# Kernel tuning notes

Hardware: AMD Instinct MI355X
Metric: run time of the kernel (lower is better)

## Reference

```python
import jax, jax.numpy as jnp
import numpy as np

N_NODES = 50000
N_EDGES = 800000
D_IN, D_H1, D_H2 = 256, 128, 64


def setup_inputs() -> dict:
    key = jax.random.key(0)
    k1, k2, k3, k4, k5, k6, k7 = jax.random.split(key, 7)
    x = jax.random.normal(k1, (N_NODES, D_IN), dtype=jnp.float32)
    edge_index = jax.random.randint(k2, (2, N_EDGES), 0, N_NODES, dtype=jnp.int64)
    edge_weight = jax.random.uniform(k3, (N_EDGES,), dtype=jnp.float32)
    # GCNConv params: Linear (no bias) weight + separate bias, Glorot-ish scale
    W1 = jax.random.normal(k4, (D_IN, D_H1), dtype=jnp.float32) / np.sqrt(D_IN)
    b1 = jnp.zeros((D_H1,), dtype=jnp.float32)
    W2 = jax.random.normal(k5, (D_H1, D_H2), dtype=jnp.float32) / np.sqrt(D_H1)
    b2 = jnp.zeros((D_H2,), dtype=jnp.float32)
    return {"x": x, "edge_index": edge_index, "edge_weight": edge_weight,
            "W1": W1, "b1": b1, "W2": W2, "b2": b2}


def _gcn_norm(edge_index, edge_weight, n_nodes):
    # PyG gcn_norm: add self-loops (weight 1), symmetric D^-1/2 A D^-1/2
    loops = jnp.arange(n_nodes, dtype=edge_index.dtype)
    src = jnp.concatenate([edge_index[0], loops])
    dst = jnp.concatenate([edge_index[1], loops])
    w = jnp.concatenate([edge_weight, jnp.ones((n_nodes,), edge_weight.dtype)])
    deg = jax.ops.segment_sum(w, dst, num_segments=n_nodes)
    dinv = jnp.where(deg > 0, jax.lax.rsqrt(deg), 0.0)
    norm = dinv[src] * w * dinv[dst]  # [E+N]
    return src, dst, norm


def _gcn_conv(h, src, dst, norm, W, b, n_nodes):
    h = h @ W                                   # [N, d_out] dense GEMM
    msg = h[src] * norm[:, None]                # gather + scale  [E+N, d_out]
    out = jax.ops.segment_sum(msg, dst, num_segments=n_nodes)  # scatter-add
    return out + b


def reference(x, edge_index, edge_weight, W1, b1, W2, b2):
    n = x.shape[0]
    src, dst, norm = _gcn_norm(edge_index, edge_weight, n)
    # dropout p=0 -> identity
    h = jax.nn.relu(_gcn_conv(x, src, dst, norm, W1, b1, n))
    h = jax.nn.relu(_gcn_conv(h, src, dst, norm, W2, b2, n))
    return h
```

## Files before the change

### kernel.cpp

```cpp
#include <hip/hip_runtime.h>


static constexpr int SCAN_CHUNK = 1024;
static constexpr int CPAD = 16;

using short8 = __attribute__((ext_vector_type(8))) short;
using f32x4  = __attribute__((ext_vector_type(4))) float;

__device__ inline unsigned short bf16rne(float f) {
  unsigned u = __float_as_uint(f);
  u += 0x7fffu + ((u >> 16) & 1u);
  return (unsigned short)(u >> 16);
}
__device__ inline float bflo(unsigned u) { return __uint_as_float(u << 16); }
__device__ inline float bfhi(unsigned u) { return __uint_as_float(u & 0xffff0000u); }

__device__ inline void wtp_pack(const float* __restrict__ W,
                                unsigned short* __restrict__ Wtp,
                                int i, int K, int C) {
  int e = i & 7;
  int l = (i >> 3) & 63;
  int rest = i >> 9;
  int NT = C / 16;
  int nt = rest % NT;
  int kc = rest / NT;
  int k = kc * 32 + (l >> 4) * 8 + e;
  int n = nt * 16 + (l & 15);
  Wtp[i] = bf16rne(W[(size_t)k * C + n]);
}

__global__ __launch_bounds__(256) void k_prep(int* __restrict__ cnt, int nz,
                                              const float* __restrict__ W1,
                                              unsigned short* __restrict__ wtp1,
                                              const float* __restrict__ W2,
                                              unsigned short* __restrict__ wtp2) {
  int i = blockIdx.x * 256 + threadIdx.x;
  if (i < nz) cnt[i] = 0;
  if (i < 256 * 128) wtp_pack(W1, wtp1, i, 256, 128);
  if (i < 128 * 64) wtp_pack(W2, wtp2, i, 128, 64);
}

__global__ __launch_bounds__(256) void k_count(const int* __restrict__ dst,
                                               int* __restrict__ cnt,
                                               int* __restrict__ epos, int E) {
  const int base = blockIdx.x * 1024 + threadIdx.x;
  int d[4];
#pragma unroll
  for (int j = 0; j < 4; ++j) {
    int e = base + j * 256;
    d[j] = (e < E) ? dst[e] : -1;
  }
#pragma unroll
  for (int j = 0; j < 4; ++j) {
    int e = base + j * 256;
    if (e < E) epos[e] = atomicAdd(&cnt[(size_t)d[j] * CPAD], 1);
  }
}

__global__ __launch_bounds__(256) void k_scan1(const int* __restrict__ in,
                                               int* __restrict__ out,
                                               int* __restrict__ sums, int n) {
  __shared__ int sd[256];
  const int base = blockIdx.x * SCAN_CHUNK;
  const int tid = threadIdx.x;
  int v[4], tot = 0;
#pragma unroll
  for (int j = 0; j < 4; ++j) {
    int idx = base + tid * 4 + j;
    v[j] = (idx < n) ? in[(size_t)idx * CPAD] : 0;
    tot += v[j];
  }
  sd[tid] = tot;
  __syncthreads();
  for (int d = 1; d < 256; d <<= 1) {
    int t = (tid >= d) ? sd[tid - d] : 0;
    __syncthreads();
    sd[tid] += t;
    __syncthreads();
  }
  if (tid == 255) sums[blockIdx.x] = sd[255];
  int run = sd[tid] - tot;
#pragma unroll
  for (int j = 0; j < 4; ++j) {
    int idx = base + tid * 4 + j;
    if (idx < n) out[idx] = run;
    run += v[j];
  }
}

__global__ __launch_bounds__(64) void k_scan2(int* __restrict__ sums, int n) {
  int tid = threadIdx.x;
  int o = (tid < n) ? sums[tid] : 0;
  int v = o;
  for (int d = 1; d < 64; d <<= 1) {
    int t = __shfl_up(v, d, 64);
    if (tid >= d) v += t;
  }
  if (tid < n) sums[tid] = v - o;
}

__global__ __launch_bounds__(256) void k_scan3(int* __restrict__ out,
                                               const int* __restrict__ sums, int n) {
  const int base = blockIdx.x * SCAN_CHUNK;
  const int add = sums[blockIdx.x];
  for (int j = threadIdx.x; j < SCAN_CHUNK; j += 256) {
    int idx = base + j;
    if (idx < n) out[idx] += add;
  }
}

__global__ __launch_bounds__(256) void k_bucket2(const int* __restrict__ src,
                                                 const int* __restrict__ dst,
                                                 const float* __restrict__ w,
                                                 const int* __restrict__ row_ptr,
                                                 const int* __restrict__ epos,
                                                 int2* __restrict__ csr, int E) {
  int e = blockIdx.x * 256 + threadIdx.x;
  if (e < E) {
    int d = dst[e];
    csr[row_ptr[d] + epos[e]] = make_int2(src[e], __float_as_int(w[e]));
  }
}

__global__ __launch_bounds__(256) void k_deg_dinv(const int* __restrict__ row_ptr,
                                                  const int2* __restrict__ csr,
                                                  float* __restrict__ dinv, int n) {
  int i = blockIdx.x * 256 + threadIdx.x;
  if (i >= n) return;
  const int e0 = row_ptr[i], e1 = row_ptr[i + 1];
  float s = 1.0f;
  int e = e0;
  for (; e + 4 <= e1; e += 4) {
    float w0 = __int_as_float(csr[e].y), w1 = __int_as_float(csr[e + 1].y);
    float w2 = __int_as_float(csr[e + 2].y), w3 = __int_as_float(csr[e + 3].y);
    s += (w0 + w1) + (w2 + w3);
  }
  for (; e < e1; ++e) s += __int_as_float(csr[e].y);
  dinv[i] = rsqrtf(s);
}

template <int K, int C, bool A_F32>
__global__ __launch_bounds__(256, A_F32 ? 3 : 4) void k_gemm_mfma(
    const void* __restrict__ Aptr, const unsigned short* __restrict__ Wtp,
    const float* __restrict__ dinv, unsigned short* __restrict__ H, int n) {
  constexpr int NT = C / 16;
  constexpr int KCH = K / 32;
  const int w = threadIdx.x >> 6;
  const int l = threadIdx.x & 63;
  const int lm = l & 15;
  const int lk = (l >> 4) * 8;
  const int row0 = (blockIdx.x * 4 + w) * 16;
  if (row0 >= n) return;
  const int m = row0 + lm;
  const bool valid = m < n;
  const size_t arow = (size_t)(valid ? m : 0) * K;

  short8 af[KCH];
  if (A_F32) {
    const float* A = (const float*)Aptr;
    float4 a[2 * KCH];
#pragma unroll
    for (int c = 0; c < KCH; ++c) {
      if (valid) {
        a[2 * c]     = *(const float4*)(A + arow + c * 32 + lk);
        a[2 * c + 1] = *(const float4*)(A + arow + c * 32 + lk + 4);
      } else {
        a[2 * c] = a[2 * c + 1] = make_float4(0.f, 0.f, 0.f, 0.f);
      }
    }
#pragma unroll
    for (int c = 0; c < KCH; ++c) {
      af[c][0] = (short)bf16rne(a[2 * c].x);     af[c][1] = (short)bf16rne(a[2 * c].y);
      af[c][2] = (short)bf16rne(a[2 * c].z);     af[c][3] = (short)bf16rne(a[2 * c].w);
      af[c][4] = (short)bf16rne(a[2 * c + 1].x); af[c][5] = (short)bf16rne(a[2 * c + 1].y);
      af[c][6] = (short)bf16rne(a[2 * c + 1].z); af[c][7] = (short)bf16rne(a[2 * c + 1].w);
    }
  } else {
    const unsigned short* A = (const unsigned short*)Aptr;
#pragma unroll
    for (int c = 0; c < KCH; ++c)
      af[c] = valid ? *(const short8*)(A + arow + c * 32 + lk)
                    : short8{0, 0, 0, 0, 0, 0, 0, 0};
  }

  f32x4 acc[NT] = {};
  const short8* B = (const short8*)Wtp;
#pragma unroll
  for (int c = 0; c < KCH; ++c)
#pragma unroll
    for (int nt = 0; nt < NT; ++nt)
      acc[nt] = __builtin_amdgcn_mfma_f32_16x16x32_bf16(af[c], B[(c * NT + nt) * 64 + l],
                                                        acc[nt], 0, 0, 0);

  const int orow = row0 + (l >> 4) * 4;
  float dv[4];
#pragma unroll
  for (int r = 0; r < 4; ++r) dv[r] = (orow + r < n) ? dinv[orow + r] : 0.f;
#pragma unroll
  for (int nt = 0; nt < NT; ++nt) {
#pragma unroll
    for (int r = 0; r < 4; ++r) {
      int g = orow + r;
      if (g < n) H[(size_t)g * C + nt * 16 + lm] = bf16rne(acc[nt][r] * dv[r]);
    }
  }
}

template <int C, bool OUTF32>
__global__ __launch_bounds__(256) void k_aggregate(
    const int* __restrict__ row_ptr, const int2* __restrict__ csr,
    const unsigned short* __restrict__ h, const float* __restrict__ dinv,
    const float* __restrict__ bias, void* __restrict__ outp, int n) {
  constexpr int LPN = C / 8;
  constexpr int NPB = 256 / LPN;
  const int g = threadIdx.x % LPN;
  const int i = blockIdx.x * NPB + threadIdx.x / LPN;
  if (i >= n) return;
  const uint4* h4 = (const uint4*)h;
  uint4 hv = h4[(size_t)i * LPN + g];
  float a0 = bflo(hv.x), a1 = bfhi(hv.x), a2 = bflo(hv.y), a3 = bfhi(hv.y);
  float a4 = bflo(hv.z), a5 = bfhi(hv.z), a6 = bflo(hv.w), a7 = bfhi(hv.w);
  const int e1 = row_ptr[i + 1];
  int e = row_ptr[i];
  for (; e + 8 <= e1; e += 8) {
    int2 c[8];
    uint4 v[8];
#pragma unroll
    for (int j = 0; j < 8; ++j) c[j] = csr[e + j];
#pragma unroll
    for (int j = 0; j < 8; ++j) v[j] = h4[(size_t)c[j].x * LPN + g];
#pragma unroll
    for (int j = 0; j < 8; ++j) {
      float wj = __int_as_float(c[j].y);
      a0 = fmaf(bflo(v[j].x), wj, a0); a1 = fmaf(bfhi(v[j].x), wj, a1);
      a2 = fmaf(bflo(v[j].y), wj, a2); a3 = fmaf(bfhi(v[j].y), wj, a3);
      a4 = fmaf(bflo(v[j].z), wj, a4); a5 = fmaf(bfhi(v[j].z), wj, a5);
      a6 = fmaf(bflo(v[j].w), wj, a6); a7 = fmaf(bfhi(v[j].w), wj, a7);
    }
  }
  for (; e + 4 <= e1; e += 4) {
    int2 c[4];
    uint4 v[4];
#pragma unroll
    for (int j = 0; j < 4; ++j) c[j] = csr[e + j];
#pragma unroll
    for (int j = 0; j < 4; ++j) v[j] = h4[(size_t)c[j].x * LPN + g];
#pragma unroll
    for (int j = 0; j < 4; ++j) {
      float wj = __int_as_float(c[j].y);
      a0 = fmaf(bflo(v[j].x), wj, a0); a1 = fmaf(bfhi(v[j].x), wj, a1);
      a2 = fmaf(bflo(v[j].y), wj, a2); a3 = fmaf(bfhi(v[j].y), wj, a3);
      a4 = fmaf(bflo(v[j].z), wj, a4); a5 = fmaf(bfhi(v[j].z), wj, a5);
      a6 = fmaf(bflo(v[j].w), wj, a6); a7 = fmaf(bfhi(v[j].w), wj, a7);
    }
  }
  for (; e < e1; ++e) {
    int2 c = csr[e];
    float wj = __int_as_float(c.y);
    uint4 v = h4[(size_t)c.x * LPN + g];
    a0 = fmaf(bflo(v.x), wj, a0); a1 = fmaf(bfhi(v.x), wj, a1);
    a2 = fmaf(bflo(v.y), wj, a2); a3 = fmaf(bfhi(v.y), wj, a3);
    a4 = fmaf(bflo(v.z), wj, a4); a5 = fmaf(bfhi(v.z), wj, a5);
    a6 = fmaf(bflo(v.w), wj, a6); a7 = fmaf(bfhi(v.w), wj, a7);
  }
  const float di = dinv[i];
  const float4* b4 = (const float4*)bias;
  float4 bb0 = b4[g * 2], bb1 = b4[g * 2 + 1];
  a0 = fmaxf(fmaf(a0, di, bb0.x), 0.f); a1 = fmaxf(fmaf(a1, di, bb0.y), 0.f);
  a2 = fmaxf(fmaf(a2, di, bb0.z), 0.f); a3 = fmaxf(fmaf(a3, di, bb0.w), 0.f);
  a4 = fmaxf(fmaf(a4, di, bb1.x), 0.f); a5 = fmaxf(fmaf(a5, di, bb1.y), 0.f);
  a6 = fmaxf(fmaf(a6, di, bb1.z), 0.f); a7 = fmaxf(fmaf(a7, di, bb1.w), 0.f);
  if (OUTF32) {
    float4* o4 = (float4*)outp;
    o4[(size_t)i * (C / 4) + g * 2]     = make_float4(a0, a1, a2, a3);
    o4[(size_t)i * (C / 4) + g * 2 + 1] = make_float4(a4, a5, a6, a7);
  } else {
    uint4 o;
    o.x = (unsigned)bf16rne(a0) | ((unsigned)bf16rne(a1) << 16);
    o.y = (unsigned)bf16rne(a2) | ((unsigned)bf16rne(a3) << 16);
    o.z = (unsigned)bf16rne(a4) | ((unsigned)bf16rne(a5) << 16);
    o.w = (unsigned)bf16rne(a6) | ((unsigned)bf16rne(a7) << 16);
    ((uint4*)outp)[(size_t)i * LPN + g] = o;
  }
}

extern "C" void kernel_launch(void* const* d_in, const int* in_sizes, int n_in,
                              void* d_out, int out_size, void* d_ws, size_t ws_size,
                              hipStream_t stream) {
  (void)n_in; (void)out_size; (void)ws_size;
  const float* x  = (const float*)d_in[0];
  const int*   ei = (const int*)d_in[1];
  const float* ew = (const float*)d_in[2];
  const float* W1 = (const float*)d_in[3];
  const float* b1 = (const float*)d_in[4];
  const float* W2 = (const float*)d_in[5];
  const float* b2 = (const float*)d_in[6];
  float* out = (float*)d_out;

  const int N = in_sizes[0] / 256;
  const int E = in_sizes[2];
  const int* src = ei;
  const int* dst = ei + E;

  float* ws      = (float*)d_ws;
  float* dinv    = ws;
  int*   row_ptr = (int*)(ws + 50176);
  int*   chunks  = row_ptr + 50176;
  int*   cnt     = chunks + 256;
  int*   epos    = cnt + 800256;
  int2*  csr     = (int2*)(epos + 800256);
  unsigned short* h1   = (unsigned short*)((int*)csr + 2 * 800256);
  unsigned short* o1   = h1 + (size_t)50000 * 128;
  unsigned short* wtp1 = o1 + (size_t)50000 * 128;
  unsigned short* wtp2 = wtp1 + 128 * 256;
  unsigned short* h2   = h1;

  const int nz = (N + 1) * CPAD;
  const int nchunks = (N + 1 + SCAN_CHUNK - 1) / SCAN_CHUNK;

  k_prep<<<(nz + 255) / 256, 256, 0, stream>>>(cnt, nz, W1, wtp1, W2, wtp2);
  k_count<<<(E + 1023) / 1024, 256, 0, stream>>>(dst, cnt, epos, E);
  k_scan1<<<nchunks, 256, 0, stream>>>(cnt, row_ptr, chunks, N + 1);
  k_scan2<<<1, 64, 0, stream>>>(chunks, nchunks);
  k_scan3<<<nchunks, 256, 0, stream>>>(row_ptr, chunks, N + 1);
  k_bucket2<<<(E + 255) / 256, 256, 0, stream>>>(src, dst, ew, row_ptr, epos, csr, E);
  k_deg_dinv<<<(N + 255) / 256, 256, 0, stream>>>(row_ptr, csr, dinv, N);

  k_gemm_mfma<256, 128, true><<<(N + 63) / 64, 256, 0, stream>>>(x, wtp1, dinv, h1, N);
  k_aggregate<128, false><<<(N + 15) / 16, 256, 0, stream>>>(row_ptr, csr, h1, dinv,
                                                             b1, o1, N);
  k_gemm_mfma<128, 64, false><<<(N + 63) / 64, 256, 0, stream>>>(o1, wtp2, dinv, h2, N);
  k_aggregate<64, true><<<(N + 31) / 32, 256, 0, stream>>>(row_ptr, csr, h2, dinv,
                                                           b2, out, N);
}
```

Before: 154.2 us.

## Fuse layer-1 GEMM into count kernel, drop scan3, fold src dinv into edge weights

The first GEMM no longer depends on dinv: its blocks are appended to the edge-count launch so the MFMA work overlaps the atomic counting. The scan's third pass is removed, and consumers instead add the per-chunk offset when reading row_ptr. A new finalize pass multiplies each CSR edge weight by dinv[src], so aggregation scales only the self term by dinv[i]. This adds a pass over all edges and an extra offset lookup per row read, in exchange for removing a launch and the dinv scaling in the GEMM epilogue.

Result: no change. 151.3 us (-1.9%).

```diff
diff --git a/kernel.cpp b/kernel.cpp
--- a/kernel.cpp
+++ b/kernel.cpp
@@ -40,21 +40,73 @@
   if (i < 128 * 64) wtp_pack(W2, wtp2, i, 128, 64);
 }
 
-__global__ __launch_bounds__(256) void k_count(const int* __restrict__ dst,
-                                               int* __restrict__ cnt,
-                                               int* __restrict__ epos, int E) {
-  const int base = blockIdx.x * 1024 + threadIdx.x;
-  int d[4];
-#pragma unroll
-  for (int j = 0; j < 4; ++j) {
-    int e = base + j * 256;
-    d[j] = (e < E) ? dst[e] : -1;
-  }
-#pragma unroll
-  for (int j = 0; j < 4; ++j) {
-    int e = base + j * 256;
-    if (e < E) epos[e] = atomicAdd(&cnt[(size_t)d[j] * CPAD], 1);
-  }
+__global__ __launch_bounds__(256, 3) void k_count_gemm1(
+    const int* __restrict__ dst, int* __restrict__ cnt, int* __restrict__ epos,
+    int E, int CB,
+    const float* __restrict__ A, const unsigned short* __restrict__ Wtp,
+    unsigned short* __restrict__ H, int n) {
+  if (blockIdx.x < CB) {
+    const int base = blockIdx.x * 1024 + threadIdx.x;
+    int d[4];
+#pragma unroll
+    for (int j = 0; j < 4; ++j) {
+      int e = base + j * 256;
+      d[j] = (e < E) ? dst[e] : -1;
+    }
+#pragma unroll
+    for (int j = 0; j < 4; ++j) {
+      int e = base + j * 256;
+      if (e < E) epos[e] = atomicAdd(&cnt[(size_t)d[j] * CPAD], 1);
+    }
+    return;
+  }
+  constexpr int K = 256, C = 128, NT = C / 16, KCH = K / 32;
+  const int w = threadIdx.x >> 6;
+  const int l = threadIdx.x & 63;
+  const int lm = l & 15;
+  const int lk = (l >> 4) * 8;
+  const int row0 = ((blockIdx.x - CB) * 4 + w) * 16;
+  if (row0 >= n) return;
+  const int m = row0 + lm;
+  const bool valid = m < n;
+  const size_t arow = (size_t)(valid ? m : 0) * K;
+
+  short8 af[KCH];
+  {
+    float4 a[2 * KCH];
+#pragma unroll
+    for (int c = 0; c < KCH; ++c) {
+      if (valid) {
+        a[2 * c]     = *(const float4*)(A + arow + c * 32 + lk);
+        a[2 * c + 1] = *(const float4*)(A + arow + c * 32 + lk + 4);
+      } else {
+        a[2 * c] = a[2 * c + 1] = make_float4(0.f, 0.f, 0.f, 0.f);
+      }
+    }
+#pragma unroll
+    for (int c = 0; c < KCH; ++c) {
+      af[c][0] = (short)bf16rne(a[2 * c].x);     af[c][1] = (short)bf16rne(a[2 * c].y);
+      af[c][2] = (short)bf16rne(a[2 * c].z);     af[c][3] = (short)bf16rne(a[2 * c].w);
+      af[c][4] = (short)bf16rne(a[2 * c + 1].x); af[c][5] = (short)bf16rne(a[2 * c + 1].y);
+      af[c][6] = (short)bf16rne(a[2 * c + 1].z); af[c][7] = (short)bf16rne(a[2 * c + 1].w);
+    }
+  }
+  f32x4 acc[NT] = {};
+  const short8* B = (const short8*)Wtp;
+#pragma unroll
+  for (int c = 0; c < KCH; ++c)
+#pragma unroll
+    for (int nt = 0; nt < NT; ++nt)
+      acc[nt] = __builtin_amdgcn_mfma_f32_16x16x32_bf16(af[c], B[(c * NT + nt) * 64 + l],
+                                                        acc[nt], 0, 0, 0);
+  const int orow = row0 + (l >> 4) * 4;
+#pragma unroll
+  for (int nt = 0; nt < NT; ++nt)
+#pragma unroll
+    for (int r = 0; r < 4; ++r) {
+      int g = orow + r;
+      if (g < n) H[(size_t)g * C + nt * 16 + lm] = bf16rne(acc[nt][r]);
+    }
 }
 
 __global__ __launch_bounds__(256) void k_scan1(const int* __restrict__ in,
@@ -99,35 +151,29 @@
   if (tid < n) sums[tid] = v - o;
 }
 
-__global__ __launch_bounds__(256) void k_scan3(int* __restrict__ out,
-                                               const int* __restrict__ sums, int n) {
-  const int base = blockIdx.x * SCAN_CHUNK;
-  const int add = sums[blockIdx.x];
-  for (int j = threadIdx.x; j < SCAN_CHUNK; j += 256) {
-    int idx = base + j;
-    if (idx < n) out[idx] += add;
-  }
-}
-
 __global__ __launch_bounds__(256) void k_bucket2(const int* __restrict__ src,
                                                  const int* __restrict__ dst,
                                                  const float* __restrict__ w,
                                                  const int* __restrict__ row_ptr,
+                                                 const int* __restrict__ chunks,
                                                  const int* __restrict__ epos,
                                                  int2* __restrict__ csr, int E) {
   int e = blockIdx.x * 256 + threadIdx.x;
   if (e < E) {
     int d = dst[e];
-    csr[row_ptr[d] + epos[e]] = make_int2(src[e], __float_as_int(w[e]));
+    int pos = row_ptr[d] + chunks[d >> 10] + epos[e];
+    csr[pos] = make_int2(src[e], __float_as_int(w[e]));
   }
 }
 
 __global__ __launch_bounds__(256) void k_deg_dinv(const int* __restrict__ row_ptr,
+                                                  const int* __restrict__ chunks,
                                                   const int2* __restrict__ csr,
                                                   float* __restrict__ dinv, int n) {
   int i = blockIdx.x * 256 + threadIdx.x;
   if (i >= n) return;
-  const int e0 = row_ptr[i], e1 = row_ptr[i + 1];
+  const int e0 = row_ptr[i] + chunks[i >> 10];
+  const int e1 = row_ptr[i + 1] + chunks[(i + 1) >> 10];
   float s = 1.0f;
   int e = e0;
   for (; e + 4 <= e1; e += 4) {
@@ -139,12 +185,22 @@
   dinv[i] = rsqrtf(s);
 }
 
-template <int K, int C, bool A_F32>
-__global__ __launch_bounds__(256, A_F32 ? 3 : 4) void k_gemm_mfma(
-    const void* __restrict__ Aptr, const unsigned short* __restrict__ Wtp,
-    const float* __restrict__ dinv, unsigned short* __restrict__ H, int n) {
-  constexpr int NT = C / 16;
-  constexpr int KCH = K / 32;
+__global__ __launch_bounds__(256) void k_finalize(int2* __restrict__ csr,
+                                                  const float* __restrict__ dinv,
+                                                  int E) {
+  int e = blockIdx.x * 256 + threadIdx.x;
+  if (e < E) {
+    int2 c = csr[e];
+    c.y = __float_as_int(__int_as_float(c.y) * dinv[c.x]);
+    csr[e] = c;
+  }
+}
+
+template <int K, int C>
+__global__ __launch_bounds__(256, 4) void k_gemm_bf(
+    const unsigned short* __restrict__ A, const unsigned short* __restrict__ Wtp,
+    unsigned short* __restrict__ H, int n) {
+  constexpr int NT = C / 16, KCH = K / 32;
   const int w = threadIdx.x >> 6;
   const int l = threadIdx.x & 63;
   const int lm = l & 15;
@@ -154,35 +210,11 @@
   const int m = row0 + lm;
   const bool valid = m < n;
   const size_t arow = (size_t)(valid ? m : 0) * K;
-
   short8 af[KCH];
-  if (A_F32) {
-    const float* A = (const float*)Aptr;
-    float4 a[2 * KCH];
-#pragma unroll
-    for (int c = 0; c < KCH; ++c) {
-      if (valid) {
-        a[2 * c]     = *(const float4*)(A + arow + c * 32 + lk);
-        a[2 * c + 1] = *(const float4*)(A + arow + c * 32 + lk + 4);
-      } else {
-        a[2 * c] = a[2 * c + 1] = make_float4(0.f, 0.f, 0.f, 0.f);
-      }
-    }
-#pragma unroll
-    for (int c = 0; c < KCH; ++c) {
-      af[c][0] = (short)bf16rne(a[2 * c].x);     af[c][1] = (short)bf16rne(a[2 * c].y);
-      af[c][2] = (short)bf16rne(a[2 * c].z);     af[c][3] = (short)bf16rne(a[2 * c].w);
-      af[c][4] = (short)bf16rne(a[2 * c + 1].x); af[c][5] = (short)bf16rne(a[2 * c + 1].y);
-      af[c][6] = (short)bf16rne(a[2 * c + 1].z); af[c][7] = (short)bf16rne(a[2 * c + 1].w);
-    }
-  } else {
-    const unsigned short* A = (const unsigned short*)Aptr;
-#pragma unroll
-    for (int c = 0; c < KCH; ++c)
-      af[c] = valid ? *(const short8*)(A + arow + c * 32 + lk)
-                    : short8{0, 0, 0, 0, 0, 0, 0, 0};
-  }
-
+#pragma unroll
+  for (int c = 0; c < KCH; ++c)
+    af[c] = valid ? *(const short8*)(A + arow + c * 32 + lk)
+                  : short8{0, 0, 0, 0, 0, 0, 0, 0};
   f32x4 acc[NT] = {};
   const short8* B = (const short8*)Wtp;
 #pragma unroll
@@ -191,37 +223,36 @@
     for (int nt = 0; nt < NT; ++nt)
       acc[nt] = __builtin_amdgcn_mfma_f32_16x16x32_bf16(af[c], B[(c * NT + nt) * 64 + l],
                                                         acc[nt], 0, 0, 0);
-
   const int orow = row0 + (l >> 4) * 4;
-  float dv[4];
-#pragma unroll
-  for (int r = 0; r < 4; ++r) dv[r] = (orow + r < n) ? dinv[orow + r] : 0.f;
-#pragma unroll
-  for (int nt = 0; nt < NT; ++nt) {
+#pragma unroll
+  for (int nt = 0; nt < NT; ++nt)
 #pragma unroll
     for (int r = 0; r < 4; ++r) {
       int g = orow + r;
-      if (g < n) H[(size_t)g * C + nt * 16 + lm] = bf16rne(acc[nt][r] * dv[r]);
-    }
-  }
+      if (g < n) H[(size_t)g * C + nt * 16 + lm] = bf16rne(acc[nt][r]);
+    }
 }
 
 template <int C, bool OUTF32>
 __global__ __launch_bounds__(256) void k_aggregate(
-    const int* __restrict__ row_ptr, const int2* __restrict__ csr,
-    const unsigned short* __restrict__ h, const float* __restrict__ dinv,
-    const float* __restrict__ bias, void* __restrict__ outp, int n) {
+    const int* __restrict__ row_ptr, const int* __restrict__ chunks,
+    const int2* __restrict__ csr, const unsigned short* __restrict__ h,
+    const float* __restrict__ dinv, const float* __restrict__ bias,
+    void* __restrict__ outp, int n) {
   constexpr int LPN = C / 8;
   constexpr int NPB = 256 / LPN;
   const int g = threadIdx.x % LPN;
   const int i = blockIdx.x * NPB + threadIdx.x / LPN;
   if (i >= n) return;
+  const float di = dinv[i];
   const uint4* h4 = (const uint4*)h;
   uint4 hv = h4[(size_t)i * LPN + g];
-  float a0 = bflo(hv.x), a1 = bfhi(hv.x), a2 = bflo(hv.y), a3 = bfhi(hv.y);
-  float a4 = bflo(hv.z), a5 = bfhi(hv.z), a6 = bflo(hv.w), a7 = bfhi(hv.w);
-  const int e1 = row_ptr[i + 1];
-  int e = row_ptr[i];
+  float a0 = di * bflo(hv.x), a1 = di * bfhi(hv.x);
+  float a2 = di * bflo(hv.y), a3 = di * bfhi(hv.y);
+  float a4 = di * bflo(hv.z), a5 = di * bfhi(hv.z);
+  float a6 = di * bflo(hv.w), a7 = di * bfhi(hv.w);
+  const int e1 = row_ptr[i + 1] + chunks[(i + 1) >> 10];
+  int e = row_ptr[i] + chunks[i >> 10];
   for (; e + 8 <= e1; e += 8) {
     int2 c[8];
     uint4 v[8];
@@ -263,7 +294,6 @@
     a4 = fmaf(bflo(v.z), wj, a4); a5 = fmaf(bfhi(v.z), wj, a5);
     a6 = fmaf(bflo(v.w), wj, a6); a7 = fmaf(bfhi(v.w), wj, a7);
   }
-  const float di = dinv[i];
   const float4* b4 = (const float4*)bias;
   float4 bb0 = b4[g * 2], bb1 = b4[g * 2 + 1];
   a0 = fmaxf(fmaf(a0, di, bb0.x), 0.f); a1 = fmaxf(fmaf(a1, di, bb0.y), 0.f);
@@ -317,19 +347,21 @@
 
   const int nz = (N + 1) * CPAD;
   const int nchunks = (N + 1 + SCAN_CHUNK - 1) / SCAN_CHUNK;
+  const int CB = (E + 1023) / 1024;
+  const int GB = (N + 63) / 64;
 
   k_prep<<<(nz + 255) / 256, 256, 0, stream>>>(cnt, nz, W1, wtp1, W2, wtp2);
-  k_count<<<(E + 1023) / 1024, 256, 0, stream>>>(dst, cnt, epos, E);
+  k_count_gemm1<<<CB + GB, 256, 0, stream>>>(dst, cnt, epos, E, CB, x, wtp1, h1, N);
   k_scan1<<<nchunks, 256, 0, stream>>>(cnt, row_ptr, chunks, N + 1);
   k_scan2<<<1, 64, 0, stream>>>(chunks, nchunks);
-  k_scan3<<<nchunks, 256, 0, stream>>>(row_ptr, chunks, N + 1);
-  k_bucket2<<<(E + 255) / 256, 256, 0, stream>>>(src, dst, ew, row_ptr, epos, csr, E);
-  k_deg_dinv<<<(N + 255) / 256, 256, 0, stream>>>(row_ptr, csr, dinv, N);
-
-  k_gemm_mfma<256, 128, true><<<(N + 63) / 64, 256, 0, stream>>>(x, wtp1, dinv, h1, N);
-  k_aggregate<128, false><<<(N + 15) / 16, 256, 0, stream>>>(row_ptr, csr, h1, dinv,
-                                                             b1, o1, N);
-  k_gemm_mfma<128, 64, false><<<(N + 63) / 64, 256, 0, stream>>>(o1, wtp2, dinv, h2, N);
-  k_aggregate<64, true><<<(N + 31) / 32, 256, 0, stream>>>(row_ptr, csr, h2, dinv,
-                                                           b2, out, N);
-}
+  k_bucket2<<<(E + 255) / 256, 256, 0, stream>>>(src, dst, ew, row_ptr, chunks,
+                                                 epos, csr, E);
+  k_deg_dinv<<<(N + 255) / 256, 256, 0, stream>>>(row_ptr, chunks, csr, dinv, N);
+  k_finalize<<<(E + 255) / 256, 256, 0, stream>>>(csr, dinv, E);
+
+  k_aggregate<128, false><<<(N + 15) / 16, 256, 0, stream>>>(row_ptr, chunks, csr,
+                                                             h1, dinv, b1, o1, N);
+  k_gemm_bf<128, 64><<<(N + 63) / 64, 256, 0, stream>>>(o1, wtp2, h2, N);
+  k_aggregate<64, true><<<(N + 31) / 32, 256, 0, stream>>>(row_ptr, chunks, csr,
+                                                           h2, dinv, b2, out, N);
+}
```
